# Optimization experiments

Hardware: AMD Instinct MI355X
Metric: run time of the kernel (lower is better)

## Reference

```python
import jax, jax.numpy as jnp
import numpy as np

B, N, F_IN = 512, 128, 133
NHID, NHEADS, HID = 64, 8, 512
FP_DIM, FP2, TASKS = 1489, 512, 12
ALPHA = 0.2
NEG_BIG = -9e15


def _lin_init(key, fan_in, fan_out):
    return jax.random.normal(key, (fan_in, fan_out), jnp.float32) / np.sqrt(fan_in)


def setup_inputs() -> dict:
    key = jax.random.key(0)
    ks = jax.random.split(key, 24)
    inp = {
        'h': jax.random.normal(ks[0], (B, N, F_IN), jnp.float32),
        'adj': jax.random.randint(ks[1], (B, N, N), 0, 2, jnp.int32),
        'edge_feat': jax.random.uniform(ks[2], (B, N, N), jnp.float32),
        'fp': jax.random.uniform(ks[3], (B, FP_DIM), jnp.float32),
        # multi-head GAT layer params (a split as [a1; a2; a_edge])
        'W_heads': jax.random.normal(ks[4], (NHEADS, F_IN, NHID), jnp.float32) / np.sqrt(F_IN),
        'a1_heads': jax.random.normal(ks[5], (NHEADS, NHID), jnp.float32) / np.sqrt(NHID),
        'a2_heads': jax.random.normal(ks[6], (NHEADS, NHID), jnp.float32) / np.sqrt(NHID),
        'ae_heads': jax.random.normal(ks[7], (NHEADS,), jnp.float32) * 0.1,
        # output GAT layer
        'W_out': jax.random.normal(ks[8], (NHID * NHEADS, HID), jnp.float32) / np.sqrt(NHID * NHEADS),
        'a1_out': jax.random.normal(ks[9], (HID,), jnp.float32) / np.sqrt(HID),
        'a2_out': jax.random.normal(ks[10], (HID,), jnp.float32) / np.sqrt(HID),
        'ae_out': jax.random.normal(ks[11], ()) * 0.1,
        # FPN
        'fc1_w': _lin_init(ks[12], FP_DIM, FP2), 'fc1_b': jnp.zeros((FP2,), jnp.float32),
        'fc2_w': _lin_init(ks[13], FP2, HID), 'fc2_b': jnp.zeros((HID,), jnp.float32),
        # cross-attention fusion
        'q_w': _lin_init(ks[14], HID, HID), 'q_b': jnp.zeros((HID,), jnp.float32),
        'k_w': _lin_init(ks[15], HID, HID), 'k_b': jnp.zeros((HID,), jnp.float32),
        'v_w': _lin_init(ks[16], HID, HID), 'v_b': jnp.zeros((HID,), jnp.float32),
        'o_w': _lin_init(ks[17], HID, HID), 'o_b': jnp.zeros((HID,), jnp.float32),
        # FFN head
        'ffn1_w': _lin_init(ks[18], HID, HID), 'ffn1_b': jnp.zeros((HID,), jnp.float32),
        'ffn2_w': _lin_init(ks[19], HID, TASKS), 'ffn2_b': jnp.zeros((TASKS,), jnp.float32),
    }
    return inp


def _leaky(x):
    return jnp.where(x >= 0, x, ALPHA * x)


def _fpgnn_forward(h, adj, edge_feat, fp,
                   W_heads, a1_heads, a2_heads, ae_heads,
                   W_out, a1_out, a2_out, ae_out,
                   fc1_w, fc1_b, fc2_w, fc2_b,
                   q_w, q_b, k_w, k_b, v_w, v_b, o_w, o_b,
                   ffn1_w, ffn1_b, ffn2_w, ffn2_b):
    mask = adj > 0  # [B,N,N]
    # --- multi-head GAT layers (concat=True) ---
    Wh = jnp.einsum('bnf,hfd->bhnd', h, W_heads)            # [B,H,N,D]
    s1 = jnp.einsum('bhnd,hd->bhn', Wh, a1_heads)
    s2 = jnp.einsum('bhnd,hd->bhn', Wh, a2_heads)
    # e[b,h,i,j] = leaky(Wh_i.a1 + Wh_j.a2 + edge_ij*ae)  (exact decomposition of
    # the original concat([Wh_i, Wh_j, edge_ij]) @ a)
    e = _leaky(s1[:, :, :, None] + s2[:, :, None, :]
               + edge_feat[:, None, :, :] * ae_heads[None, :, None, None])
    att = jnp.where(mask[:, None], e, NEG_BIG)
    att = jax.nn.softmax(att, axis=-1)                       # softmax over dim=1 of [N,N]
    hp = jnp.einsum('bhij,bhjd->bhid', att, Wh)
    x = jax.nn.elu(hp)                                       # concat=True -> ELU
    x = jnp.transpose(x, (0, 2, 1, 3)).reshape(B, N, NHEADS * NHID)
    # --- output GAT layer (concat=False) ---
    Wx = x @ W_out                                           # [B,N,HID]
    t1 = Wx @ a1_out                                         # [B,N]
    t2 = Wx @ a2_out
    e2 = _leaky(t1[:, :, None] + t2[:, None, :] + edge_feat * ae_out)
    att2 = jnp.where(mask, e2, NEG_BIG)
    att2 = jax.nn.softmax(att2, axis=-1)
    hp2 = jnp.einsum('bij,bjd->bid', att2, Wx)
    gat_nodes = jax.nn.elu(hp2)                              # F.elu in GATOne
    gat_out = gat_nodes.mean(axis=1)                         # molecule readout [B,HID]
    # --- FPN ---
    fpn_out = jax.nn.relu(fp @ fc1_w + fc1_b) @ fc2_w + fc2_b  # [B,HID]
    # --- cross-attention fusion ---
    q = gat_out @ q_w + q_b
    k = fpn_out @ k_w + k_b
    v = fpn_out @ v_w + v_b
    score = jnp.sum(q * k, axis=-1, keepdims=True) / np.sqrt(HID)  # [B,1]
    weight = jax.nn.softmax(score[:, :, None], axis=-1)[:, :, 0]    # softmax over size-1 dim -> ones
    fused = q + weight * v
    fused = jax.nn.relu(fused @ o_w + o_b)
    # --- FFN head (dropout p=0, eval) ---
    out = jax.nn.relu(fused @ ffn1_w + ffn1_b) @ ffn2_w + ffn2_b
    return out


def reference(h, adj, edge_feat, fp,
              W_heads, a1_heads, a2_heads, ae_heads,
              W_out, a1_out, a2_out, ae_out,
              fc1_w, fc1_b, fc2_w, fc2_b,
              q_w, q_b, k_w, k_b, v_w, v_b, o_w, o_b,
              ffn1_w, ffn1_b, ffn2_w, ffn2_b):
    return _fpgnn_forward(h, adj, edge_feat, fp,
                          W_heads, a1_heads, a2_heads, ae_heads,
                          W_out, a1_out, a2_out, ae_out,
                          fc1_w, fc1_b, fc2_w, fc2_b,
                          q_w, q_b, k_w, k_b, v_w, v_b, o_w, o_b,
                          ffn1_w, ffn1_b, ffn2_w, ffn2_b)
```

## Files before the change

kernel.cpp:

```cpp
#include <hip/hip_runtime.h>
#include <hip/hip_bf16.h>


#define ALPHA_LK 0.2f
#define LOG2E 1.44269504f
#define KP1 192
#define KPF 1536
#define MINF_BF16 0xFF80u

typedef unsigned short ushort_t;
typedef __attribute__((ext_vector_type(8))) short bfrag;
typedef __attribute__((ext_vector_type(4))) float ffrag;

__device__ __forceinline__ float b2f(ushort_t u) {
  return __uint_as_float(((unsigned)u) << 16);
}
__device__ __forceinline__ ushort_t f2b(float f) {
  unsigned u = __float_as_uint(f);
  unsigned r = (u + 0x7fffu + ((u >> 16) & 1u)) >> 16;
  return (ushort_t)r;
}
__device__ __forceinline__ unsigned cvt_pk(float lo, float hi) {
  unsigned r;
  asm("v_cvt_pk_bf16_f32 %0, %1, %2" : "=v"(r) : "v"(lo), "v"(hi));
  return r;
}
__device__ __forceinline__ float frcp(float x) {
  float r;
  asm("v_rcp_f32 %0, %1" : "=v"(r) : "v"(x));
  return r;
}
__device__ __forceinline__ float fexp2(float x) {
#if __has_builtin(__builtin_amdgcn_exp2f)
  return __builtin_amdgcn_exp2f(x);
#else
  return exp2f(x);
#endif
}
__device__ __forceinline__ float elu1(float v) {
  return v > 0.f ? v : __expf(v) - 1.f;
}

__device__ __forceinline__ void gll16(const void* g, void* l) {
  __builtin_amdgcn_global_load_lds(
      (const __attribute__((address_space(1))) unsigned int*)(unsigned long long)g,
      (__attribute__((address_space(3))) unsigned int*)(unsigned long long)l,
      16, 0, 0);
}

__global__ __launch_bounds__(256) void repack_h(const float* __restrict__ h,
                                                ushort_t* __restrict__ hb) {
  int o = blockIdx.x * 256 + threadIdx.x;
  int row = o / 48, c4 = (o - row * 48) * 4;
  const float* hr = h + (size_t)row * 133;
  ushort4 v;
  v.x = (c4 + 0 < 133) ? f2b(hr[c4 + 0]) : (ushort_t)0;
  v.y = (c4 + 1 < 133) ? f2b(hr[c4 + 1]) : (ushort_t)0;
  v.z = (c4 + 2 < 133) ? f2b(hr[c4 + 2]) : (ushort_t)0;
  v.w = (c4 + 3 < 133) ? f2b(hr[c4 + 3]) : (ushort_t)0;
  *(ushort4*)&hb[(size_t)row * KP1 + c4] = v;
}

__global__ __launch_bounds__(256) void repack_fp(const float* __restrict__ fp,
                                                 ushort_t* __restrict__ fpb) {
  int o = blockIdx.x * 256 + threadIdx.x;
  int row = o / 384, c4 = (o - row * 384) * 4;
  const float* fr = fp + (size_t)row * 1489;
  ushort4 v;
  v.x = (c4 + 0 < 1489) ? f2b(fr[c4 + 0]) : (ushort_t)0;
  v.y = (c4 + 1 < 1489) ? f2b(fr[c4 + 1]) : (ushort_t)0;
  v.z = (c4 + 2 < 1489) ? f2b(fr[c4 + 2]) : (ushort_t)0;
  v.w = (c4 + 3 < 1489) ? f2b(fr[c4 + 3]) : (ushort_t)0;
  *(ushort4*)&fpb[(size_t)row * KPF + c4] = v;
}

__global__ __launch_bounds__(256) void repack_w2t(const float* __restrict__ Whd,
                                                  ushort_t* __restrict__ W2t) {
  int o = blockIdx.x * 256 + threadIdx.x;
  if (o >= 512 * 48) return;
  int col = o / 48, c4 = (o - col * 48) * 4;
  int hh = col >> 6, d = col & 63;
  ushort4 v;
  v.x = (c4 + 0 < 133) ? f2b(Whd[(hh * 133 + c4 + 0) * 64 + d]) : (ushort_t)0;
  v.y = (c4 + 1 < 133) ? f2b(Whd[(hh * 133 + c4 + 1) * 64 + d]) : (ushort_t)0;
  v.z = (c4 + 2 < 133) ? f2b(Whd[(hh * 133 + c4 + 2) * 64 + d]) : (ushort_t)0;
  v.w = (c4 + 3 < 133) ? f2b(Whd[(hh * 133 + c4 + 3) * 64 + d]) : (ushort_t)0;
  *(ushort4*)&W2t[(size_t)col * KP1 + c4] = v;
}

__global__ __launch_bounds__(256) void repack_t(const float* __restrict__ W,
                                                ushort_t* __restrict__ Wt,
                                                int K, int N, int Kpad) {
  int kp4 = Kpad >> 2;
  int o = blockIdx.x * 256 + threadIdx.x;
  if (o >= N * kp4) return;
  int col = o / kp4, k4 = (o - col * kp4) * 4;
  ushort4 v;
  v.x = (k4 + 0 < K) ? f2b(W[(size_t)(k4 + 0) * N + col]) : (ushort_t)0;
  v.y = (k4 + 1 < K) ? f2b(W[(size_t)(k4 + 1) * N + col]) : (ushort_t)0;
  v.z = (k4 + 2 < K) ? f2b(W[(size_t)(k4 + 2) * N + col]) : (ushort_t)0;
  v.w = (k4 + 3 < K) ? f2b(W[(size_t)(k4 + 3) * N + col]) : (ushort_t)0;
  *(ushort4*)&Wt[(size_t)col * Kpad + k4] = v;
}

__global__ __launch_bounds__(256) void repack_t7(
    const float* __restrict__ w0, const float* __restrict__ w1,
    const float* __restrict__ w2, const float* __restrict__ w3,
    const float* __restrict__ w4, const float* __restrict__ w5,
    const float* __restrict__ qb, const float* __restrict__ vb,
    ushort_t* __restrict__ d0, ushort_t* __restrict__ d1,
    ushort_t* __restrict__ d2, ushort_t* __restrict__ d3,
    ushort_t* __restrict__ d4, ushort_t* __restrict__ d5,
    float* __restrict__ qvb) {
  int y = blockIdx.y;
  int o = blockIdx.x * 256 + threadIdx.x;
  if (y == 6) {
    if (o < 512) qvb[o] = qb[o] + vb[o];
    return;
  }
  const float* W = y == 0 ? w0 : y == 1 ? w1 : y == 2 ? w2
                 : y == 3 ? w3 : y == 4 ? w4 : w5;
  ushort_t* Wt = y == 0 ? d0 : y == 1 ? d1 : y == 2 ? d2
               : y == 3 ? d3 : y == 4 ? d4 : d5;
  int col = o >> 7, k4 = (o & 127) * 4;
  ushort4 v;
  v.x = f2b(W[(size_t)(k4 + 0) * 512 + col]);
  v.y = f2b(W[(size_t)(k4 + 1) * 512 + col]);
  v.z = f2b(W[(size_t)(k4 + 2) * 512 + col]);
  v.w = f2b(W[(size_t)(k4 + 3) * 512 + col]);
  *(ushort4*)&Wt[(size_t)col * 512 + k4] = v;
}

__global__ __launch_bounds__(256) void repack_em(const float* __restrict__ edge,
                                                 const int* __restrict__ adj,
                                                 ushort_t* __restrict__ em) {
  size_t o = ((size_t)blockIdx.x * 256 + threadIdx.x) * 4;
  float4 e = *(const float4*)&edge[o];
  int4 a = *(const int4*)&adj[o];
  ushort4 v;
  v.x = a.x > 0 ? f2b(e.x) : (ushort_t)MINF_BF16;
  v.y = a.y > 0 ? f2b(e.y) : (ushort_t)MINF_BF16;
  v.z = a.z > 0 ? f2b(e.z) : (ushort_t)MINF_BF16;
  v.w = a.w > 0 ? f2b(e.w) : (ushort_t)MINF_BF16;
  *(ushort4*)&em[o] = v;
}

__global__ __launch_bounds__(256) void wa12_kernel(
    const float* __restrict__ W, const float* __restrict__ a1,
    const float* __restrict__ a2, float* __restrict__ wa1,
    float* __restrict__ wa2) {
  int wv = threadIdx.x >> 6, lane = threadIdx.x & 63;
  int k = blockIdx.x * 4 + wv;
  const float* wr = W + (size_t)k * 512;
  float p1 = 0.f, p2 = 0.f;
#pragma unroll
  for (int i = 0; i < 8; ++i) {
    float v = wr[lane + i * 64];
    p1 += v * a1[lane + i * 64];
    p2 += v * a2[lane + i * 64];
  }
#pragma unroll
  for (int off = 32; off; off >>= 1) {
    p1 += __shfl_down(p1, off);
    p2 += __shfl_down(p2, off);
  }
  if (lane == 0) { wa1[k] = p1; wa2[k] = p2; }
}

__global__ __launch_bounds__(256) void t12x_kernel(
    const ushort_t* __restrict__ xb, const float* __restrict__ wa1,
    const float* __restrict__ wa2, float* __restrict__ t1o,
    float* __restrict__ t2o, int base) {
  int wv = threadIdx.x >> 6, lane = threadIdx.x & 63;
  int row = blockIdx.x * 4 + wv;
  const ushort_t* xr = xb + (size_t)row * 512;
  ushort4 u0 = *(const ushort4*)&xr[lane * 8];
  ushort4 u1 = *(const ushort4*)&xr[lane * 8 + 4];
  float xv[8] = {b2f(u0.x), b2f(u0.y), b2f(u0.z), b2f(u0.w),
                 b2f(u1.x), b2f(u1.y), b2f(u1.z), b2f(u1.w)};
  float p1 = 0.f, p2 = 0.f;
#pragma unroll
  for (int i = 0; i < 8; ++i) {
    p1 += xv[i] * wa1[lane * 8 + i];
    p2 += xv[i] * wa2[lane * 8 + i];
  }
#pragma unroll
  for (int off = 32; off; off >>= 1) {
    p1 += __shfl_down(p1, off);
    p2 += __shfl_down(p2, off);
  }
  if (lane == 0) {
    t1o[base * 128 + row] = p1;
    t2o[base * 128 + row] = p2;
  }
}

__global__ __launch_bounds__(256) void att2_kernel(
    const ushort_t* __restrict__ em, const float* __restrict__ t1,
    const float* __restrict__ t2, const float* __restrict__ aeo,
    ushort_t* __restrict__ awg, float* __restrict__ sinvg, int base) {
  __shared__ float t2s[128];
  const int bl = blockIdx.x >> 1, bg = base + bl;
  const int rb = (blockIdx.x & 1) * 64;
  const int t = threadIdx.x;
  if (t < 128) t2s[t] = t2[(size_t)bg * 128 + t] * LOG2E;
  __syncthreads();
  const int row = rb + (t >> 2), qtr = t & 3;
  const float ae2 = aeo[0] * LOG2E;
  const float rt1 = t1[(size_t)bg * 128 + row] * LOG2E;
  const ushort_t* emr = em + (size_t)bg * 16384 + row * 128 + qtr * 32;
  ushort_t* awr = awg + (size_t)bl * 16384 + row * 128 + qtr * 32;
  float s = 0.f;
#pragma unroll
  for (int v = 0; v < 4; ++v) {
    uint4 eu = *(const uint4*)&emr[v * 8];
    const unsigned uu[4] = {eu.x, eu.y, eu.z, eu.w};
    unsigned po[4];
#pragma unroll
    for (int pr = 0; pr < 4; ++pr) {
      float elo = __uint_as_float(uu[pr] << 16);
      float ehi = __uint_as_float(uu[pr] & 0xffff0000u);
      float e0 = fmaf(elo, ae2, rt1 + t2s[qtr * 32 + v * 8 + pr * 2]);
      float e1 = fmaf(ehi, ae2, rt1 + t2s[qtr * 32 + v * 8 + pr * 2 + 1]);
      e0 = fmaxf(e0, ALPHA_LK * e0);
      e1 = fmaxf(e1, ALPHA_LK * e1);
      float p0 = (elo != -INFINITY) ? fexp2(e0) : 0.f;
      float p1 = (ehi != -INFINITY) ? fexp2(e1) : 0.f;
      unsigned q = cvt_pk(p0, p1);
      po[pr] = q;
      s += __uint_as_float(q << 16) + __uint_as_float(q & 0xffff0000u);
    }
    *(uint4*)&awr[v * 8] = make_uint4(po[0], po[1], po[2], po[3]);
  }
  s += __shfl_xor(s, 1);
  s += __shfl_xor(s, 2);
  if (qtr == 0) sinvg[(size_t)bl * 128 + row] = 1.f / fmaxf(s, 1e-30f);
}

__global__ __launch_bounds__(256) void fused_gat1(
    const ushort_t* __restrict__ hb, const ushort_t* __restrict__ W2t,
    const ushort_t* __restrict__ edgeM, const float* __restrict__ a1h,
    const float* __restrict__ a2h, const float* __restrict__ ae,
    ushort_t* __restrict__ x, int base) {
  __shared__ union {
    struct { ushort_t As[128][64]; ushort_t Bs[64][64]; } g;
    ushort_t WS[64][136];
  } u;
  __shared__ float ss1[128], ss2[128];
  const int id = blockIdx.x;
  const int hh = (id >> 3) & 7;
  const int bl = ((id >> 6) << 3) | (id & 7);
  const int bg = base + bl;
  const int t = threadIdx.x;
  const int lane = t & 63, w = t >> 6;
  const int l16 = lane & 15, quad = lane >> 4;
  const int w8 = w * 8, sr8 = (t >> 3) & 7;
  const int csw = ((t & 7) ^ sr8) << 3;

  const ushort_t* gA = hb + (size_t)(bl * 128 + w8 + sr8) * KP1 + csw;
  const ushort_t* gB = W2t + (size_t)(hh * 64 + w8 + sr8) * KP1 + csw;
  ffrag acc[2][4];
#pragma unroll
  for (int mi = 0; mi < 2; ++mi)
#pragma unroll
    for (int ni = 0; ni < 4; ++ni) acc[mi][ni] = {0.f, 0.f, 0.f, 0.f};
  for (int k0 = 0; k0 < KP1; k0 += 64) {
    __syncthreads();
#pragma unroll
    for (int p = 0; p < 4; ++p)
      gll16(gA + (size_t)(p * 32) * KP1 + k0, &u.g.As[p * 32 + w8][0]);
#pragma unroll
    for (int p = 0; p < 2; ++p)
      gll16(gB + (size_t)(p * 32) * KP1 + k0, &u.g.Bs[p * 32 + w8][0]);
    __syncthreads();
#pragma unroll
    for (int ks = 0; ks < 2; ++ks) {
      const int cs = ((ks * 4 + quad) ^ (l16 & 7)) << 3;
      bfrag af[2], bf[4];
#pragma unroll
      for (int mi = 0; mi < 2; ++mi)
        af[mi] = *(const bfrag*)&u.g.As[w * 32 + mi * 16 + l16][cs];
#pragma unroll
      for (int ni = 0; ni < 4; ++ni)
        bf[ni] = *(const bfrag*)&u.g.Bs[ni * 16 + l16][cs];
#pragma unroll
      for (int mi = 0; mi < 2; ++mi)
#pragma unroll
        for (int ni = 0; ni < 4; ++ni)
          acc[mi][ni] = __builtin_amdgcn_mfma_f32_16x16x32_bf16(
              af[mi], bf[ni], acc[mi][ni], 0, 0, 0);
    }
  }
  __syncthreads();

#pragma unroll
  for (int mi = 0; mi < 2; ++mi)
#pragma unroll
    for (int ni = 0; ni < 4; ++ni) {
      int col = ni * 16 + l16;
      int rowb = w * 32 + mi * 16 + quad * 4;
      uint2 pv;
      pv.x = cvt_pk(acc[mi][ni][0], acc[mi][ni][1]);
      pv.y = cvt_pk(acc[mi][ni][2], acc[mi][ni][3]);
      *(uint2*)&u.WS[col][rowb] = pv;
    }
  __syncthreads();

  uint4 ereg[2][4];
  {
    const ushort_t* em = edgeM + (size_t)bg * 16384;
#pragma unroll
    for (int mi = 0; mi < 2; ++mi) {
      int row = w * 32 + mi * 16 + l16;
#pragma unroll
      for (int ks = 0; ks < 4; ++ks)
        ereg[mi][ks] = *(const uint4*)&em[row * 128 + ks * 32 + quad * 8];
    }
  }
  {
    int n = t & 127;
    const float* av = (t < 128) ? a1h : a2h;
    float p = 0.f;
#pragma unroll 8
    for (int d = 0; d < 64; ++d) p += b2f(u.WS[d][n]) * av[hh * 64 + d];
    p *= LOG2E;
    if (t < 128) ss1[n] = p; else ss2[n] = p;
  }
  __syncthreads();

  const float aeh2 = ae[hh] * LOG2E;
  float rs1[2];
  rs1[0] = ss1[w * 32 + l16];
  rs1[1] = ss1[w * 32 + 16 + l16];
  uint4 aw[2][4];
#pragma unroll
  for (int mi = 0; mi < 2; ++mi) {
#pragma unroll
    for (int ks = 0; ks < 4; ++ks) {
      float s2v[8];
      *(float4*)&s2v[0] = *(const float4*)&ss2[ks * 32 + quad * 8];
      *(float4*)&s2v[4] = *(const float4*)&ss2[ks * 32 + quad * 8 + 4];
      const unsigned uu[4] = {ereg[mi][ks].x, ereg[mi][ks].y,
                              ereg[mi][ks].z, ereg[mi][ks].w};
      unsigned po[4];
#pragma unroll
      for (int pr = 0; pr < 4; ++pr) {
        float elo = __uint_as_float(uu[pr] << 16);
        float ehi = __uint_as_float(uu[pr] & 0xffff0000u);
        float e0 = fmaf(elo, aeh2, rs1[mi] + s2v[pr * 2]);
        float e1 = fmaf(ehi, aeh2, rs1[mi] + s2v[pr * 2 + 1]);
        e0 = fmaxf(e0, ALPHA_LK * e0);
        e1 = fmaxf(e1, ALPHA_LK * e1);
        float p0 = (elo != -INFINITY) ? fexp2(e0) : 0.f;
        float p1 = (ehi != -INFINITY) ? fexp2(e1) : 0.f;
        po[pr] = cvt_pk(p0, p1);
      }
      aw[mi][ks] = make_uint4(po[0], po[1], po[2], po[3]);
    }
  }

  bfrag bones;
#pragma unroll
  for (int i = 0; i < 8; ++i) bones[i] = (short)0x3F80;

  ffrag acc2[2][4];
  ffrag accs[2];
#pragma unroll
  for (int mi = 0; mi < 2; ++mi) {
    accs[mi] = {0.f, 0.f, 0.f, 0.f};
#pragma unroll
    for (int ni = 0; ni < 4; ++ni) acc2[mi][ni] = {0.f, 0.f, 0.f, 0.f};
  }
#pragma unroll
  for (int ks = 0; ks < 4; ++ks) {
    bfrag bfr[4];
#pragma unroll
    for (int ni = 0; ni < 4; ++ni)
      bfr[ni] = *(const bfrag*)&u.WS[ni * 16 + l16][ks * 32 + quad * 8];
#pragma unroll
    for (int mi = 0; mi < 2; ++mi) {
      bfrag afr;
      __builtin_memcpy(&afr, &aw[mi][ks], 16);
#pragma unroll
      for (int ni = 0; ni < 4; ++ni)
        acc2[mi][ni] = __builtin_amdgcn_mfma_f32_16x16x32_bf16(
            afr, bfr[ni], acc2[mi][ni], 0, 0, 0);
      accs[mi] = __builtin_amdgcn_mfma_f32_16x16x32_bf16(
          afr, bones, accs[mi], 0, 0, 0);
    }
  }
  float sv[2][4];
#pragma unroll
  for (int mi = 0; mi < 2; ++mi)
#pragma unroll
    for (int r = 0; r < 4; ++r)
      sv[mi][r] = frcp(fmaxf(accs[mi][r], 1e-30f));

#pragma unroll
  for (int mi = 0; mi < 2; ++mi)
#pragma unroll
    for (int ni = 0; ni < 4; ++ni) {
      float e0 = elu1(acc2[mi][ni][0] * sv[mi][0]);
      float e1 = elu1(acc2[mi][ni][1] * sv[mi][1]);
      float e2 = elu1(acc2[mi][ni][2] * sv[mi][2]);
      float e3 = elu1(acc2[mi][ni][3] * sv[mi][3]);
      unsigned p01 = cvt_pk(e0, e1), p23 = cvt_pk(e2, e3);
      int rl = w * 32 + mi * 16 + quad * 4;
      size_t bo = (size_t)(bl * 128 + rl) * 512 + hh * 64 + ni * 16 + l16;
      x[bo] = (ushort_t)p01;
      x[bo + 512] = (ushort_t)(p01 >> 16);
      x[bo + 1024] = (ushort_t)p23;
      x[bo + 1536] = (ushort_t)(p23 >> 16);
    }
}

__global__ __launch_bounds__(256) void fused_gat2(
    const ushort_t* __restrict__ xb, const ushort_t* __restrict__ Wot,
    const ushort_t* __restrict__ awg, const float* __restrict__ sinvg,
    ushort_t* __restrict__ gatb, int base) {
  __shared__ union {
    struct { ushort_t As[128][64]; ushort_t Bs[128][64]; } g;
    ushort_t WS[128][136];
  } u;
  __shared__ float ps[4][64];
  const int id = blockIdx.x;
  const int sp2 = (id >> 3) & 3;
  const int bl = ((id >> 5) << 3) | (id & 7);
  const int bg = base + bl;
  const int t = threadIdx.x;
  const int lane = t & 63, w = t >> 6;
  const int wm = w >> 1, wn = w & 1;
  const int l16 = lane & 15, quad = lane >> 4;
  const int w8 = w * 8, sr8 = (t >> 3) & 7;
  const int csw = ((t & 7) ^ sr8) << 3;

  const ushort_t* gA = xb + (size_t)(bl * 128 + w8 + sr8) * 512 + csw;
  const ushort_t* gB = Wot + (size_t)(sp2 * 128 + w8 + sr8) * 512 + csw;
  ffrag acc[4][4];
#pragma unroll
  for (int mi = 0; mi < 4; ++mi)
#pragma unroll
    for (int ni = 0; ni < 4; ++ni) acc[mi][ni] = {0.f, 0.f, 0.f, 0.f};
  for (int k0 = 0; k0 < 512; k0 += 64) {
    __syncthreads();
#pragma unroll
    for (int p = 0; p < 4; ++p) {
      gll16(gA + (size_t)(p * 32) * 512 + k0, &u.g.As[p * 32 + w8][0]);
      gll16(gB + (size_t)(p * 32) * 512 + k0, &u.g.Bs[p * 32 + w8][0]);
    }
    __syncthreads();
#pragma unroll
    for (int ks = 0; ks < 2; ++ks) {
      const int cs = ((ks * 4 + quad) ^ (l16 & 7)) << 3;
      bfrag af[4], bf[4];
#pragma unroll
      for (int i = 0; i < 4; ++i) {
        af[i] = *(const bfrag*)&u.g.As[wm * 64 + i * 16 + l16][cs];
        bf[i] = *(const bfrag*)&u.g.Bs[wn * 64 + i * 16 + l16][cs];
      }
#pragma unroll
      for (int mi = 0; mi < 4; ++mi)
#pragma unroll
        for (int ni = 0; ni < 4; ++ni)
          acc[mi][ni] = __builtin_amdgcn_mfma_f32_16x16x32_bf16(
              af[mi], bf[ni], acc[mi][ni], 0, 0, 0);
    }
  }
  __syncthreads();

#pragma unroll
  for (int mi = 0; mi < 4; ++mi)
#pragma unroll
    for (int ni = 0; ni < 4; ++ni) {
      int col = wn * 64 + ni * 16 + l16;
      int rowb = wm * 64 + mi * 16 + quad * 4;
      uint2 pv;
      pv.x = cvt_pk(acc[mi][ni][0], acc[mi][ni][1]);
      pv.y = cvt_pk(acc[mi][ni][2], acc[mi][ni][3]);
      *(uint2*)&u.WS[col][rowb] = pv;
    }
  __syncthreads();

  uint4 awf[2][4];
  float sv[2][4];
  {
    const ushort_t* ap = awg + (size_t)bl * 16384;
#pragma unroll
    for (int mi = 0; mi < 2; ++mi) {
      int row = w * 32 + mi * 16 + l16;
#pragma unroll
      for (int ks = 0; ks < 4; ++ks)
        awf[mi][ks] = *(const uint4*)&ap[row * 128 + ks * 32 + quad * 8];
      float si = sinvg[(size_t)bl * 128 + row];
#pragma unroll
      for (int r = 0; r < 4; ++r) sv[mi][r] = __shfl(si, quad * 4 + r);
    }
  }

  for (int s0 = 0; s0 < 2; ++s0) {
    ffrag acc2[2][4];
#pragma unroll
    for (int mi = 0; mi < 2; ++mi)
#pragma unroll
      for (int ni = 0; ni < 4; ++ni) acc2[mi][ni] = {0.f, 0.f, 0.f, 0.f};
#pragma unroll
    for (int ks = 0; ks < 4; ++ks) {
      bfrag bfr[4];
#pragma unroll
      for (int ni = 0; ni < 4; ++ni)
        bfr[ni] = *(const bfrag*)&u.WS[s0 * 64 + ni * 16 + l16][ks * 32 + quad * 8];
#pragma unroll
      for (int mi = 0; mi < 2; ++mi) {
        bfrag afr;
        __builtin_memcpy(&afr, &awf[mi][ks], 16);
#pragma unroll
        for (int ni = 0; ni < 4; ++ni)
          acc2[mi][ni] = __builtin_amdgcn_mfma_f32_16x16x32_bf16(
              afr, bfr[ni], acc2[mi][ni], 0, 0, 0);
      }
    }
    __syncthreads();
#pragma unroll
    for (int ni = 0; ni < 4; ++ni) {
      float s = 0.f;
#pragma unroll
      for (int mi = 0; mi < 2; ++mi)
#pragma unroll
        for (int r = 0; r < 4; ++r) s += elu1(acc2[mi][ni][r] * sv[mi][r]);
      s += __shfl_xor(s, 16);
      s += __shfl_xor(s, 32);
      if (quad == 0) ps[w][ni * 16 + l16] = s;
    }
    __syncthreads();
    if (t < 64) {
      float s = ps[0][t] + ps[1][t] + ps[2][t] + ps[3][t];
      gatb[(size_t)bg * 512 + sp2 * 128 + s0 * 64 + t] = f2b(s * (1.f / 128.f));
    }
  }
}

__device__ __forceinline__ void tail_kloop(
    const ushort_t* __restrict__ A, const ushort_t* __restrict__ Bt,
    int K, int ld, ushort_t (*As)[64], ushort_t (*Bs)[64],
    ffrag (*acc)[4], int row0, int col0, int t) {
  const int lane = t & 63, w = t >> 6;
  const int wm = w >> 1, wn = w & 1;
  const int l16 = lane & 15, quad = lane >> 4;
  const int w8 = w * 8, sr8 = (t >> 3) & 7;
  const int csw = ((t & 7) ^ sr8) << 3;
  const ushort_t* gA = A + (size_t)(row0 + w8 + sr8) * ld + csw;
  const ushort_t* gB = Bt + (size_t)(col0 + w8 + sr8) * ld + csw;
  for (int k0 = 0; k0 < K; k0 += 64) {
    __syncthreads();
#pragma unroll
    for (int p = 0; p < 4; ++p) {
      gll16(gA + (size_t)(p * 32) * ld + k0, &As[p * 32 + w8][0]);
      gll16(gB + (size_t)(p * 32) * ld + k0, &Bs[p * 32 + w8][0]);
    }
    __syncthreads();
#pragma unroll
    for (int ks = 0; ks < 2; ++ks) {
      const int cs = ((ks * 4 + quad) ^ (l16 & 7)) << 3;
      bfrag af[4], bf[4];
#pragma unroll
      for (int i = 0; i < 4; ++i) {
        af[i] = *(const bfrag*)&As[wm * 64 + i * 16 + l16][cs];
        bf[i] = *(const bfrag*)&Bs[wn * 64 + i * 16 + l16][cs];
      }
#pragma unroll
      for (int mi = 0; mi < 4; ++mi)
#pragma unroll
        for (int ni = 0; ni < 4; ++ni)
          acc[mi][ni] = __builtin_amdgcn_mfma_f32_16x16x32_bf16(
              af[mi], bf[ni], acc[mi][ni], 0, 0, 0);
    }
  }
}

template <int DUAL, int RELU>
__global__ __launch_bounds__(256) void gemm_tail(
    const ushort_t* __restrict__ A1, const ushort_t* __restrict__ Bt1,
    int K1, int ld1,
    const ushort_t* __restrict__ A2, const ushort_t* __restrict__ Bt2,
    const float* __restrict__ bias, ushort_t* __restrict__ C) {
  __shared__ ushort_t As[128][64];
  __shared__ ushort_t Bs[128][64];
  const int t = threadIdx.x;
  const int lane = t & 63, w = t >> 6;
  const int wm = w >> 1, wn = w & 1;
  const int l16 = lane & 15, quad = lane >> 4;
  const int row0 = blockIdx.y * 128, col0 = blockIdx.x * 128;

  ffrag acc[4][4];
#pragma unroll
  for (int mi = 0; mi < 4; ++mi)
#pragma unroll
    for (int ni = 0; ni < 4; ++ni) acc[mi][ni] = {0.f, 0.f, 0.f, 0.f};

  tail_kloop(A1, Bt1, K1, ld1, As, Bs, acc, row0, col0, t);
  if (DUAL) tail_kloop(A2, Bt2, 512, 512, As, Bs, acc, row0, col0, t);

#pragma unroll
  for (int mi = 0; mi < 4; ++mi)
#pragma unroll
    for (int ni = 0; ni < 4; ++ni) {
      int col = col0 + wn * 64 + ni * 16 + l16;
      float bb = bias[col];
      float v0 = acc[mi][ni][0] + bb, v1 = acc[mi][ni][1] + bb;
      float v2 = acc[mi][ni][2] + bb, v3 = acc[mi][ni][3] + bb;
      if (RELU) {
        v0 = fmaxf(v0, 0.f); v1 = fmaxf(v1, 0.f);
        v2 = fmaxf(v2, 0.f); v3 = fmaxf(v3, 0.f);
      }
      unsigned p01 = cvt_pk(v0, v1), p23 = cvt_pk(v2, v3);
      int row = row0 + wm * 64 + mi * 16 + quad * 4;
      size_t o = (size_t)row * 512 + col;
      C[o] = (ushort_t)p01;
      C[o + 512] = (ushort_t)(p01 >> 16);
      C[o + 1024] = (ushort_t)p23;
      C[o + 1536] = (ushort_t)(p23 >> 16);
    }
}

__global__ __launch_bounds__(256) void ffn2_kernel(
    const ushort_t* __restrict__ f5, const float* __restrict__ W,
    const float* __restrict__ b, float* __restrict__ out) {
  int wv = threadIdx.x >> 6, lane = threadIdx.x & 63;
  int row = blockIdx.x * 4 + wv;
  const ushort_t* fr = f5 + (size_t)row * 512;
  float v[8];
  ushort4 u0 = *(const ushort4*)&fr[lane * 8];
  ushort4 u1 = *(const ushort4*)&fr[lane * 8 + 4];
  v[0] = b2f(u0.x); v[1] = b2f(u0.y); v[2] = b2f(u0.z); v[3] = b2f(u0.w);
  v[4] = b2f(u1.x); v[5] = b2f(u1.y); v[6] = b2f(u1.z); v[7] = b2f(u1.w);
#pragma unroll
  for (int j = 0; j < 12; ++j) {
    float s = 0.f;
#pragma unroll
    for (int i = 0; i < 8; ++i) s += v[i] * W[(size_t)(lane * 8 + i) * 12 + j];
#pragma unroll
    for (int off = 32; off; off >>= 1) s += __shfl_down(s, off);
    if (lane == 0) out[(size_t)row * 12 + j] = s + b[j];
  }
}

extern "C" void kernel_launch(void* const* d_in, const int* in_sizes, int n_in,
                              void* d_out, int out_size, void* d_ws, size_t ws_size,
                              hipStream_t stream) {
  const float* h        = (const float*)d_in[0];
  const int*   adj      = (const int*)d_in[1];
  const float* edge     = (const float*)d_in[2];
  const float* fp       = (const float*)d_in[3];
  const float* W_heads  = (const float*)d_in[4];
  const float* a1_heads = (const float*)d_in[5];
  const float* a2_heads = (const float*)d_in[6];
  const float* ae_heads = (const float*)d_in[7];
  const float* W_out  = (const float*)d_in[8];
  const float* a1_out = (const float*)d_in[9];
  const float* a2_out = (const float*)d_in[10];
  const float* ae_out = (const float*)d_in[11];
  const float* fc1_w = (const float*)d_in[12];
  const float* fc1_b = (const float*)d_in[13];
  const float* fc2_w = (const float*)d_in[14];
  const float* fc2_b = (const float*)d_in[15];
  const float* q_w = (const float*)d_in[16];
  const float* q_b = (const float*)d_in[17];
  const float* v_w = (const float*)d_in[20];
  const float* v_b = (const float*)d_in[21];
  const float* o_w = (const float*)d_in[22];
  const float* o_b = (const float*)d_in[23];
  const float* ffn1_w = (const float*)d_in[24];
  const float* ffn1_b = (const float*)d_in[25];
  const float* ffn2_w = (const float*)d_in[26];
  const float* ffn2_b = (const float*)d_in[27];
  float* out = (float*)d_out;

  const size_t hb_bytes = (size_t)65536 * KP1 * 2;
  const size_t em_bytes = (size_t)512 * 16384 * 2;
  const size_t tail_bytes =
      (size_t)512 * KPF * 2 * 2 + (size_t)512 * 512 * 2 * 12 + 2048;
  const size_t fixed_bytes = hb_bytes + em_bytes + (size_t)512 * KP1 * 2 +
                             (size_t)2 * 65536 * 4 + tail_bytes + 16384;
  int C = 32;
  for (int cand = 512; cand >= 32; cand >>= 1) {
    size_t need = (size_t)cand * (131072 + 32768 + 512) + fixed_bytes;
    if (need <= ws_size) { C = cand; break; }
  }
  const int M = C * 128;

  char* p = (char*)d_ws;
  ushort_t* xb  = (ushort_t*)p; p += (size_t)C * 65536 * 2;
  ushort_t* awg = (ushort_t*)p; p += (size_t)C * 16384 * 2;
  float* sinv   = (float*)p;    p += (size_t)C * 128 * 4;
  ushort_t* hb  = (ushort_t*)p; p += hb_bytes;
  ushort_t* em  = (ushort_t*)p; p += em_bytes;
  ushort_t* W2t = (ushort_t*)p; p += (size_t)512 * KP1 * 2;
  float* t1 = (float*)p; p += 65536 * 4;
  float* t2 = (float*)p; p += 65536 * 4;
  ushort_t* fpb  = (ushort_t*)p; p += (size_t)512 * KPF * 2;
  ushort_t* fc1t = (ushort_t*)p; p += (size_t)512 * KPF * 2;
  ushort_t* Wot  = (ushort_t*)p; p += (size_t)512 * 512 * 2;
  ushort_t* fc2t = (ushort_t*)p; p += (size_t)512 * 512 * 2;
  ushort_t* qwt  = (ushort_t*)p; p += (size_t)512 * 512 * 2;
  ushort_t* vwt  = (ushort_t*)p; p += (size_t)512 * 512 * 2;
  ushort_t* owt  = (ushort_t*)p; p += (size_t)512 * 512 * 2;
  ushort_t* f1t  = (ushort_t*)p; p += (size_t)512 * 512 * 2;
  ushort_t* gatb = (ushort_t*)p; p += (size_t)512 * 512 * 2;
  ushort_t* fb1  = (ushort_t*)p; p += (size_t)512 * 512 * 2;
  ushort_t* fb2  = (ushort_t*)p; p += (size_t)512 * 512 * 2;
  ushort_t* fb3  = (ushort_t*)p; p += (size_t)512 * 512 * 2;
  ushort_t* fb4  = (ushort_t*)p; p += (size_t)512 * 512 * 2;
  ushort_t* fb5  = (ushort_t*)p; p += (size_t)512 * 512 * 2;
  float* qvb = (float*)p; p += 2048;
  float* wa1 = (float*)p; p += 2048;
  float* wa2 = (float*)p; p += 2048;

  repack_h<<<12288, 256, 0, stream>>>(h, hb);
  repack_em<<<8192, 256, 0, stream>>>(edge, adj, em);
  repack_w2t<<<96, 256, 0, stream>>>(W_heads, W2t);
  repack_fp<<<768, 256, 0, stream>>>(fp, fpb);
  repack_t<<<768, 256, 0, stream>>>(fc1_w, fc1t, 1489, 512, KPF);
  repack_t7<<<dim3(256, 7), 256, 0, stream>>>(
      W_out, fc2_w, q_w, v_w, o_w, ffn1_w, q_b, v_b,
      Wot, fc2t, qwt, vwt, owt, f1t, qvb);
  wa12_kernel<<<128, 256, 0, stream>>>(W_out, a1_out, a2_out, wa1, wa2);

  for (int base = 0; base < 512; base += C) {
    fused_gat1<<<8 * C, 256, 0, stream>>>(
        hb + (size_t)base * 128 * KP1, W2t, em, a1_heads, a2_heads,
        ae_heads, xb, base);
    t12x_kernel<<<M / 4, 256, 0, stream>>>(xb, wa1, wa2, t1, t2, base);
    att2_kernel<<<2 * C, 256, 0, stream>>>(em, t1, t2, ae_out, awg, sinv, base);
    fused_gat2<<<4 * C, 256, 0, stream>>>(xb, Wot, awg, sinv, gatb, base);
  }

  gemm_tail<0, 1><<<dim3(4, 4), 256, 0, stream>>>(
      fpb, fc1t, KPF, KPF, nullptr, nullptr, fc1_b, fb1);
  gemm_tail<0, 0><<<dim3(4, 4), 256, 0, stream>>>(
      fb1, fc2t, 512, 512, nullptr, nullptr, fc2_b, fb2);
  gemm_tail<1, 0><<<dim3(4, 4), 256, 0, stream>>>(
      gatb, qwt, 512, 512, fb2, vwt, qvb, fb3);
  gemm_tail<0, 1><<<dim3(4, 4), 256, 0, stream>>>(
      fb3, owt, 512, 512, nullptr, nullptr, o_b, fb4);
  gemm_tail<0, 1><<<dim3(4, 4), 256, 0, stream>>>(
      fb4, f1t, 512, 512, nullptr, nullptr, ffn1_b, fb5);
  ffn2_kernel<<<128, 256, 0, stream>>>(fb5, ffn2_w, ffn2_b, out);
}
```

Baseline: 461.0 us.

## Merge prep kernels, fold attention projections into MFMA, fuse t12 into att2

All repack and weight-prep kernels become a single prep_all launch dispatched by block index. The layer-1 attention scores now come from an extra MFMA column built from W·a1 and W·a2, which are precomputed and stored as bf16. This replaces the per-thread post-GEMM dot products over the bf16 output tile. The t1/t2 projection kernel is fused into the layer-2 attention kernel, which removes launches and a global round trip. The costs are one block per graph in att2t, which gives less parallelism, and some precision loss because the folded attention vectors are rounded to bf16.

```diff
diff --git a/kernel.cpp b/kernel.cpp
--- a/kernel.cpp
+++ b/kernel.cpp
@@ -48,171 +48,199 @@
       16, 0, 0);
 }
 
-__global__ __launch_bounds__(256) void repack_h(const float* __restrict__ h,
-                                                ushort_t* __restrict__ hb) {
-  int o = blockIdx.x * 256 + threadIdx.x;
-  int row = o / 48, c4 = (o - row * 48) * 4;
-  const float* hr = h + (size_t)row * 133;
-  ushort4 v;
-  v.x = (c4 + 0 < 133) ? f2b(hr[c4 + 0]) : (ushort_t)0;
-  v.y = (c4 + 1 < 133) ? f2b(hr[c4 + 1]) : (ushort_t)0;
-  v.z = (c4 + 2 < 133) ? f2b(hr[c4 + 2]) : (ushort_t)0;
-  v.w = (c4 + 3 < 133) ? f2b(hr[c4 + 3]) : (ushort_t)0;
-  *(ushort4*)&hb[(size_t)row * KP1 + c4] = v;
-}
-
-__global__ __launch_bounds__(256) void repack_fp(const float* __restrict__ fp,
-                                                 ushort_t* __restrict__ fpb) {
-  int o = blockIdx.x * 256 + threadIdx.x;
-  int row = o / 384, c4 = (o - row * 384) * 4;
-  const float* fr = fp + (size_t)row * 1489;
-  ushort4 v;
-  v.x = (c4 + 0 < 1489) ? f2b(fr[c4 + 0]) : (ushort_t)0;
-  v.y = (c4 + 1 < 1489) ? f2b(fr[c4 + 1]) : (ushort_t)0;
-  v.z = (c4 + 2 < 1489) ? f2b(fr[c4 + 2]) : (ushort_t)0;
-  v.w = (c4 + 3 < 1489) ? f2b(fr[c4 + 3]) : (ushort_t)0;
-  *(ushort4*)&fpb[(size_t)row * KPF + c4] = v;
-}
-
-__global__ __launch_bounds__(256) void repack_w2t(const float* __restrict__ Whd,
-                                                  ushort_t* __restrict__ W2t) {
-  int o = blockIdx.x * 256 + threadIdx.x;
-  if (o >= 512 * 48) return;
-  int col = o / 48, c4 = (o - col * 48) * 4;
-  int hh = col >> 6, d = col & 63;
-  ushort4 v;
-  v.x = (c4 + 0 < 133) ? f2b(Whd[(hh * 133 + c4 + 0) * 64 + d]) : (ushort_t)0;
-  v.y = (c4 + 1 < 133) ? f2b(Whd[(hh * 133 + c4 + 1) * 64 + d]) : (ushort_t)0;
-  v.z = (c4 + 2 < 133) ? f2b(Whd[(hh * 133 + c4 + 2) * 64 + d]) : (ushort_t)0;
-  v.w = (c4 + 3 < 133) ? f2b(Whd[(hh * 133 + c4 + 3) * 64 + d]) : (ushort_t)0;
-  *(ushort4*)&W2t[(size_t)col * KP1 + c4] = v;
-}
-
-__global__ __launch_bounds__(256) void repack_t(const float* __restrict__ W,
-                                                ushort_t* __restrict__ Wt,
-                                                int K, int N, int Kpad) {
-  int kp4 = Kpad >> 2;
-  int o = blockIdx.x * 256 + threadIdx.x;
-  if (o >= N * kp4) return;
-  int col = o / kp4, k4 = (o - col * kp4) * 4;
-  ushort4 v;
-  v.x = (k4 + 0 < K) ? f2b(W[(size_t)(k4 + 0) * N + col]) : (ushort_t)0;
-  v.y = (k4 + 1 < K) ? f2b(W[(size_t)(k4 + 1) * N + col]) : (ushort_t)0;
-  v.z = (k4 + 2 < K) ? f2b(W[(size_t)(k4 + 2) * N + col]) : (ushort_t)0;
-  v.w = (k4 + 3 < K) ? f2b(W[(size_t)(k4 + 3) * N + col]) : (ushort_t)0;
-  *(ushort4*)&Wt[(size_t)col * Kpad + k4] = v;
-}
-
-__global__ __launch_bounds__(256) void repack_t7(
-    const float* __restrict__ w0, const float* __restrict__ w1,
-    const float* __restrict__ w2, const float* __restrict__ w3,
-    const float* __restrict__ w4, const float* __restrict__ w5,
+__global__ __launch_bounds__(256) void prep_all(
+    const float* __restrict__ h, const int* __restrict__ adj,
+    const float* __restrict__ edge, const float* __restrict__ fp,
+    const float* __restrict__ Whd, const float* __restrict__ a1h,
+    const float* __restrict__ a2h,
+    const float* __restrict__ W_out, const float* __restrict__ a1o,
+    const float* __restrict__ a2o,
+    const float* __restrict__ fc1_w, const float* __restrict__ fc2_w,
+    const float* __restrict__ q_w, const float* __restrict__ v_w,
+    const float* __restrict__ o_w, const float* __restrict__ ffn1_w,
     const float* __restrict__ qb, const float* __restrict__ vb,
-    ushort_t* __restrict__ d0, ushort_t* __restrict__ d1,
-    ushort_t* __restrict__ d2, ushort_t* __restrict__ d3,
-    ushort_t* __restrict__ d4, ushort_t* __restrict__ d5,
-    float* __restrict__ qvb) {
-  int y = blockIdx.y;
-  int o = blockIdx.x * 256 + threadIdx.x;
-  if (y == 6) {
-    if (o < 512) qvb[o] = qb[o] + vb[o];
+    ushort_t* __restrict__ hb, ushort_t* __restrict__ em,
+    ushort_t* __restrict__ W2t, ushort_t* __restrict__ fpb,
+    ushort_t* __restrict__ fc1t,
+    ushort_t* __restrict__ Wot, ushort_t* __restrict__ fc2t,
+    ushort_t* __restrict__ qwt, ushort_t* __restrict__ vwt,
+    ushort_t* __restrict__ owt, ushort_t* __restrict__ f1t,
+    float* __restrict__ wa1, float* __restrict__ wa2,
+    ushort_t* __restrict__ wh12, float* __restrict__ qvb) {
+  int bid = blockIdx.x;
+  const int t = threadIdx.x;
+
+  if (bid < 8) {
+    int hh = bid;
+    if (t < 192) {
+      float s1 = 0.f, s2 = 0.f;
+      if (t < 133) {
+        const float* wr = Whd + (size_t)(hh * 133 + t) * 64;
+        const float* a1r = a1h + hh * 64;
+        const float* a2r = a2h + hh * 64;
+#pragma unroll 8
+        for (int d = 0; d < 64; ++d) {
+          float wv = wr[d];
+          s1 += wv * a1r[d];
+          s2 += wv * a2r[d];
+        }
+      }
+      wh12[hh * 384 + t] = f2b(s1);
+      wh12[hh * 384 + 192 + t] = f2b(s2);
+    }
     return;
   }
-  const float* W = y == 0 ? w0 : y == 1 ? w1 : y == 2 ? w2
-                 : y == 3 ? w3 : y == 4 ? w4 : w5;
-  ushort_t* Wt = y == 0 ? d0 : y == 1 ? d1 : y == 2 ? d2
-               : y == 3 ? d3 : y == 4 ? d4 : d5;
-  int col = o >> 7, k4 = (o & 127) * 4;
-  ushort4 v;
-  v.x = f2b(W[(size_t)(k4 + 0) * 512 + col]);
-  v.y = f2b(W[(size_t)(k4 + 1) * 512 + col]);
-  v.z = f2b(W[(size_t)(k4 + 2) * 512 + col]);
-  v.w = f2b(W[(size_t)(k4 + 3) * 512 + col]);
-  *(ushort4*)&Wt[(size_t)col * 512 + k4] = v;
-}
-
-__global__ __launch_bounds__(256) void repack_em(const float* __restrict__ edge,
-                                                 const int* __restrict__ adj,
-                                                 ushort_t* __restrict__ em) {
-  size_t o = ((size_t)blockIdx.x * 256 + threadIdx.x) * 4;
-  float4 e = *(const float4*)&edge[o];
-  int4 a = *(const int4*)&adj[o];
-  ushort4 v;
-  v.x = a.x > 0 ? f2b(e.x) : (ushort_t)MINF_BF16;
-  v.y = a.y > 0 ? f2b(e.y) : (ushort_t)MINF_BF16;
-  v.z = a.z > 0 ? f2b(e.z) : (ushort_t)MINF_BF16;
-  v.w = a.w > 0 ? f2b(e.w) : (ushort_t)MINF_BF16;
-  *(ushort4*)&em[o] = v;
-}
-
-__global__ __launch_bounds__(256) void wa12_kernel(
-    const float* __restrict__ W, const float* __restrict__ a1,
-    const float* __restrict__ a2, float* __restrict__ wa1,
-    float* __restrict__ wa2) {
-  int wv = threadIdx.x >> 6, lane = threadIdx.x & 63;
-  int k = blockIdx.x * 4 + wv;
-  const float* wr = W + (size_t)k * 512;
-  float p1 = 0.f, p2 = 0.f;
-#pragma unroll
-  for (int i = 0; i < 8; ++i) {
-    float v = wr[lane + i * 64];
-    p1 += v * a1[lane + i * 64];
-    p2 += v * a2[lane + i * 64];
-  }
-#pragma unroll
-  for (int off = 32; off; off >>= 1) {
-    p1 += __shfl_down(p1, off);
-    p2 += __shfl_down(p2, off);
-  }
-  if (lane == 0) { wa1[k] = p1; wa2[k] = p2; }
-}
-
-__global__ __launch_bounds__(256) void t12x_kernel(
-    const ushort_t* __restrict__ xb, const float* __restrict__ wa1,
-    const float* __restrict__ wa2, float* __restrict__ t1o,
-    float* __restrict__ t2o, int base) {
-  int wv = threadIdx.x >> 6, lane = threadIdx.x & 63;
-  int row = blockIdx.x * 4 + wv;
-  const ushort_t* xr = xb + (size_t)row * 512;
-  ushort4 u0 = *(const ushort4*)&xr[lane * 8];
-  ushort4 u1 = *(const ushort4*)&xr[lane * 8 + 4];
-  float xv[8] = {b2f(u0.x), b2f(u0.y), b2f(u0.z), b2f(u0.w),
-                 b2f(u1.x), b2f(u1.y), b2f(u1.z), b2f(u1.w)};
-  float p1 = 0.f, p2 = 0.f;
-#pragma unroll
-  for (int i = 0; i < 8; ++i) {
-    p1 += xv[i] * wa1[lane * 8 + i];
-    p2 += xv[i] * wa2[lane * 8 + i];
-  }
-#pragma unroll
-  for (int off = 32; off; off >>= 1) {
-    p1 += __shfl_down(p1, off);
-    p2 += __shfl_down(p2, off);
-  }
-  if (lane == 0) {
-    t1o[base * 128 + row] = p1;
-    t2o[base * 128 + row] = p2;
-  }
-}
-
-__global__ __launch_bounds__(256) void att2_kernel(
-    const ushort_t* __restrict__ em, const float* __restrict__ t1,
-    const float* __restrict__ t2, const float* __restrict__ aeo,
+  bid -= 8;
+  if (bid < 128) {
+    int wv = t >> 6, lane = t & 63;
+    int k = bid * 4 + wv;
+    const float* wr = W_out + (size_t)k * 512;
+    float p1 = 0.f, p2 = 0.f;
+#pragma unroll
+    for (int i = 0; i < 8; ++i) {
+      float v = wr[lane + i * 64];
+      p1 += v * a1o[lane + i * 64];
+      p2 += v * a2o[lane + i * 64];
+    }
+#pragma unroll
+    for (int off = 32; off; off >>= 1) {
+      p1 += __shfl_down(p1, off);
+      p2 += __shfl_down(p2, off);
+    }
+    if (lane == 0) { wa1[k] = p1; wa2[k] = p2; }
+    return;
+  }
+  bid -= 128;
+  if (bid < 2) {
+    int o = bid * 256 + t;
+    qvb[o] = qb[o] + vb[o];
+    return;
+  }
+  bid -= 2;
+  if (bid < 96) {
+    int o = bid * 256 + t;
+    if (o < 512 * 48) {
+      int col = o / 48, c4 = (o - col * 48) * 4;
+      int hh = col >> 6, d = col & 63;
+      ushort4 v;
+      v.x = (c4 + 0 < 133) ? f2b(Whd[(hh * 133 + c4 + 0) * 64 + d]) : (ushort_t)0;
+      v.y = (c4 + 1 < 133) ? f2b(Whd[(hh * 133 + c4 + 1) * 64 + d]) : (ushort_t)0;
+      v.z = (c4 + 2 < 133) ? f2b(Whd[(hh * 133 + c4 + 2) * 64 + d]) : (ushort_t)0;
+      v.w = (c4 + 3 < 133) ? f2b(Whd[(hh * 133 + c4 + 3) * 64 + d]) : (ushort_t)0;
+      *(ushort4*)&W2t[(size_t)col * KP1 + c4] = v;
+    }
+    return;
+  }
+  bid -= 96;
+  if (bid < 768) {
+    int o = bid * 256 + t;
+    int row = o / 384, c4 = (o - row * 384) * 4;
+    const float* fr = fp + (size_t)row * 1489;
+    ushort4 v;
+    v.x = (c4 + 0 < 1489) ? f2b(fr[c4 + 0]) : (ushort_t)0;
+    v.y = (c4 + 1 < 1489) ? f2b(fr[c4 + 1]) : (ushort_t)0;
+    v.z = (c4 + 2 < 1489) ? f2b(fr[c4 + 2]) : (ushort_t)0;
+    v.w = (c4 + 3 < 1489) ? f2b(fr[c4 + 3]) : (ushort_t)0;
+    *(ushort4*)&fpb[(size_t)row * KPF + c4] = v;
+    return;
+  }
+  bid -= 768;
+  if (bid < 768) {
+    int o = bid * 256 + t;
+    int col = o / 384, k4 = (o - col * 384) * 4;
+    ushort4 v;
+    v.x = (k4 + 0 < 1489) ? f2b(fc1_w[(size_t)(k4 + 0) * 512 + col]) : (ushort_t)0;
+    v.y = (k4 + 1 < 1489) ? f2b(fc1_w[(size_t)(k4 + 1) * 512 + col]) : (ushort_t)0;
+    v.z = (k4 + 2 < 1489) ? f2b(fc1_w[(size_t)(k4 + 2) * 512 + col]) : (ushort_t)0;
+    v.w = (k4 + 3 < 1489) ? f2b(fc1_w[(size_t)(k4 + 3) * 512 + col]) : (ushort_t)0;
+    *(ushort4*)&fc1t[(size_t)col * KPF + k4] = v;
+    return;
+  }
+  bid -= 768;
+  if (bid < 1536) {
+    int y = bid >> 8;
+    int o = (bid & 255) * 256 + t;
+    const float* W = y == 0 ? W_out : y == 1 ? fc2_w : y == 2 ? q_w
+                   : y == 3 ? v_w : y == 4 ? o_w : ffn1_w;
+    ushort_t* Wt = y == 0 ? Wot : y == 1 ? fc2t : y == 2 ? qwt
+                 : y == 3 ? vwt : y == 4 ? owt : f1t;
+    int col = o >> 7, k4 = (o & 127) * 4;
+    ushort4 v;
+    v.x = f2b(W[(size_t)(k4 + 0) * 512 + col]);
+    v.y = f2b(W[(size_t)(k4 + 1) * 512 + col]);
+    v.z = f2b(W[(size_t)(k4 + 2) * 512 + col]);
+    v.w = f2b(W[(size_t)(k4 + 3) * 512 + col]);
+    *(ushort4*)&Wt[(size_t)col * 512 + k4] = v;
+    return;
+  }
+  bid -= 1536;
+  if (bid < 12288) {
+    int o = bid * 256 + t;
+    int row = o / 48, c4 = (o - row * 48) * 4;
+    const float* hr = h + (size_t)row * 133;
+    ushort4 v;
+    v.x = (c4 + 0 < 133) ? f2b(hr[c4 + 0]) : (ushort_t)0;
+    v.y = (c4 + 1 < 133) ? f2b(hr[c4 + 1]) : (ushort_t)0;
+    v.z = (c4 + 2 < 133) ? f2b(hr[c4 + 2]) : (ushort_t)0;
+    v.w = (c4 + 3 < 133) ? f2b(hr[c4 + 3]) : (ushort_t)0;
+    *(ushort4*)&hb[(size_t)row * KP1 + c4] = v;
+    return;
+  }
+  bid -= 12288;
+  {
+    size_t o = ((size_t)bid * 256 + t) * 4;
+    float4 e = *(const float4*)&edge[o];
+    int4 a = *(const int4*)&adj[o];
+    ushort4 v;
+    v.x = a.x > 0 ? f2b(e.x) : (ushort_t)MINF_BF16;
+    v.y = a.y > 0 ? f2b(e.y) : (ushort_t)MINF_BF16;
+    v.z = a.z > 0 ? f2b(e.z) : (ushort_t)MINF_BF16;
+    v.w = a.w > 0 ? f2b(e.w) : (ushort_t)MINF_BF16;
+    *(ushort4*)&em[o] = v;
+  }
+}
+
+__global__ __launch_bounds__(256) void att2t(
+    const ushort_t* __restrict__ xb, const ushort_t* __restrict__ em,
+    const float* __restrict__ wa1, const float* __restrict__ wa2,
+    const float* __restrict__ aeo,
     ushort_t* __restrict__ awg, float* __restrict__ sinvg, int base) {
-  __shared__ float t2s[128];
-  const int bl = blockIdx.x >> 1, bg = base + bl;
-  const int rb = (blockIdx.x & 1) * 64;
+  __shared__ float t1s[128], t2s[128];
+  __shared__ float was1[512], was2[512];
+  const int bl = blockIdx.x, bg = base + bl;
   const int t = threadIdx.x;
-  if (t < 128) t2s[t] = t2[(size_t)bg * 128 + t] * LOG2E;
+  was1[t] = wa1[t]; was1[t + 256] = wa1[t + 256];
+  was2[t] = wa2[t]; was2[t + 256] = wa2[t + 256];
   __syncthreads();
-  const int row = rb + (t >> 2), qtr = t & 3;
+  const int row = t >> 1, half = t & 1;
+  {
+    const ushort_t* xr = xb + (size_t)(bl * 128 + row) * 512 + half * 256;
+    float p1 = 0.f, p2 = 0.f;
+#pragma unroll 4
+    for (int i = 0; i < 32; ++i) {
+      uint4 u = *(const uint4*)&xr[i * 8];
+      const unsigned uu[4] = {u.x, u.y, u.z, u.w};
+#pragma unroll
+      for (int pr = 0; pr < 4; ++pr) {
+        float lo = __uint_as_float(uu[pr] << 16);
+        float hi = __uint_as_float(uu[pr] & 0xffff0000u);
+        int c = half * 256 + i * 8 + pr * 2;
+        p1 = fmaf(lo, was1[c], p1); p1 = fmaf(hi, was1[c + 1], p1);
+        p2 = fmaf(lo, was2[c], p2); p2 = fmaf(hi, was2[c + 1], p2);
+      }
+    }
+    p1 += __shfl_xor(p1, 1);
+    p2 += __shfl_xor(p2, 1);
+    if (!half) { t1s[row] = p1 * LOG2E; t2s[row] = p2 * LOG2E; }
+  }
+  __syncthreads();
   const float ae2 = aeo[0] * LOG2E;
-  const float rt1 = t1[(size_t)bg * 128 + row] * LOG2E;
-  const ushort_t* emr = em + (size_t)bg * 16384 + row * 128 + qtr * 32;
-  ushort_t* awr = awg + (size_t)bl * 16384 + row * 128 + qtr * 32;
+  const float rt1 = t1s[row];
+  const ushort_t* emr = em + (size_t)bg * 16384 + row * 128 + half * 64;
+  ushort_t* awr = awg + (size_t)bl * 16384 + row * 128 + half * 64;
   float s = 0.f;
 #pragma unroll
-  for (int v = 0; v < 4; ++v) {
+  for (int v = 0; v < 8; ++v) {
     uint4 eu = *(const uint4*)&emr[v * 8];
     const unsigned uu[4] = {eu.x, eu.y, eu.z, eu.w};
     unsigned po[4];
@@ -220,8 +248,8 @@
     for (int pr = 0; pr < 4; ++pr) {
       float elo = __uint_as_float(uu[pr] << 16);
       float ehi = __uint_as_float(uu[pr] & 0xffff0000u);
-      float e0 = fmaf(elo, ae2, rt1 + t2s[qtr * 32 + v * 8 + pr * 2]);
-      float e1 = fmaf(ehi, ae2, rt1 + t2s[qtr * 32 + v * 8 + pr * 2 + 1]);
+      float e0 = fmaf(elo, ae2, rt1 + t2s[half * 64 + v * 8 + pr * 2]);
+      float e1 = fmaf(ehi, ae2, rt1 + t2s[half * 64 + v * 8 + pr * 2 + 1]);
       e0 = fmaxf(e0, ALPHA_LK * e0);
       e1 = fmaxf(e1, ALPHA_LK * e1);
       float p0 = (elo != -INFINITY) ? fexp2(e0) : 0.f;
@@ -233,20 +261,20 @@
     *(uint4*)&awr[v * 8] = make_uint4(po[0], po[1], po[2], po[3]);
   }
   s += __shfl_xor(s, 1);
-  s += __shfl_xor(s, 2);
-  if (qtr == 0) sinvg[(size_t)bl * 128 + row] = 1.f / fmaxf(s, 1e-30f);
+  if (!half) sinvg[(size_t)bl * 128 + row] = 1.f / fmaxf(s, 1e-30f);
 }
 
 __global__ __launch_bounds__(256) void fused_gat1(
     const ushort_t* __restrict__ hb, const ushort_t* __restrict__ W2t,
-    const ushort_t* __restrict__ edgeM, const float* __restrict__ a1h,
-    const float* __restrict__ a2h, const float* __restrict__ ae,
+    const ushort_t* __restrict__ edgeM, const ushort_t* __restrict__ wh12g,
+    const float* __restrict__ ae,
     ushort_t* __restrict__ x, int base) {
   __shared__ union {
     struct { ushort_t As[128][64]; ushort_t Bs[64][64]; } g;
     ushort_t WS[64][136];
   } u;
   __shared__ float ss1[128], ss2[128];
+  __shared__ ushort_t wh12s[2][192];
   const int id = blockIdx.x;
   const int hh = (id >> 3) & 7;
   const int bl = ((id >> 6) << 3) | (id & 7);
@@ -257,13 +285,20 @@
   const int w8 = w * 8, sr8 = (t >> 3) & 7;
   const int csw = ((t & 7) ^ sr8) << 3;
 
+  if (t < 96)
+    *(ushort4*)&(&wh12s[0][0])[t * 4] =
+        *(const ushort4*)&wh12g[hh * 384 + t * 4];
+
   const ushort_t* gA = hb + (size_t)(bl * 128 + w8 + sr8) * KP1 + csw;
   const ushort_t* gB = W2t + (size_t)(hh * 64 + w8 + sr8) * KP1 + csw;
   ffrag acc[2][4];
-#pragma unroll
-  for (int mi = 0; mi < 2; ++mi)
+  ffrag acc_s[2];
+#pragma unroll
+  for (int mi = 0; mi < 2; ++mi) {
+    acc_s[mi] = {0.f, 0.f, 0.f, 0.f};
 #pragma unroll
     for (int ni = 0; ni < 4; ++ni) acc[mi][ni] = {0.f, 0.f, 0.f, 0.f};
+  }
   for (int k0 = 0; k0 < KP1; k0 += 64) {
     __syncthreads();
 #pragma unroll
@@ -277,6 +312,9 @@
     for (int ks = 0; ks < 2; ++ks) {
       const int cs = ((ks * 4 + quad) ^ (l16 & 7)) << 3;
       bfrag af[2], bf[4];
+      bfrag bs = {0, 0, 0, 0, 0, 0, 0, 0};
+      if (l16 < 2)
+        bs = *(const bfrag*)&wh12s[l16][k0 + ks * 32 + quad * 8];
 #pragma unroll
       for (int mi = 0; mi < 2; ++mi)
         af[mi] = *(const bfrag*)&u.g.As[w * 32 + mi * 16 + l16][cs];
@@ -284,11 +322,14 @@
       for (int ni = 0; ni < 4; ++ni)
         bf[ni] = *(const bfrag*)&u.g.Bs[ni * 16 + l16][cs];
 #pragma unroll
-      for (int mi = 0; mi < 2; ++mi)
+      for (int mi = 0; mi < 2; ++mi) {
 #pragma unroll
         for (int ni = 0; ni < 4; ++ni)
           acc[mi][ni] = __builtin_amdgcn_mfma_f32_16x16x32_bf16(
               af[mi], bf[ni], acc[mi][ni], 0, 0, 0);
+        acc_s[mi] = __builtin_amdgcn_mfma_f32_16x16x32_bf16(
+            af[mi], bs, acc_s[mi], 0, 0, 0);
+      }
     }
   }
   __syncthreads();
@@ -304,8 +345,14 @@
       pv.y = cvt_pk(acc[mi][ni][2], acc[mi][ni][3]);
       *(uint2*)&u.WS[col][rowb] = pv;
     }
-  __syncthreads();
-
+  if (l16 < 2) {
+    float* sp = (l16 == 0) ? ss1 : ss2;
+#pragma unroll
+    for (int mi = 0; mi < 2; ++mi)
+#pragma unroll
+      for (int r = 0; r < 4; ++r)
+        sp[w * 32 + mi * 16 + quad * 4 + r] = acc_s[mi][r] * LOG2E;
+  }
   uint4 ereg[2][4];
   {
     const ushort_t* em = edgeM + (size_t)bg * 16384;
@@ -316,15 +363,6 @@
       for (int ks = 0; ks < 4; ++ks)
         ereg[mi][ks] = *(const uint4*)&em[row * 128 + ks * 32 + quad * 8];
     }
-  }
-  {
-    int n = t & 127;
-    const float* av = (t < 128) ? a1h : a2h;
-    float p = 0.f;
-#pragma unroll 8
-    for (int d = 0; d < 64; ++d) p += b2f(u.WS[d][n]) * av[hh * 64 + d];
-    p *= LOG2E;
-    if (t < 128) ss1[n] = p; else ss2[n] = p;
   }
   __syncthreads();
 
@@ -687,6 +725,7 @@
     if (need <= ws_size) { C = cand; break; }
   }
   const int M = C * 128;
+  (void)M;
 
   char* p = (char*)d_ws;
   ushort_t* xb  = (ushort_t*)p; p += (size_t)C * 65536 * 2;
@@ -695,8 +734,9 @@
   ushort_t* hb  = (ushort_t*)p; p += hb_bytes;
   ushort_t* em  = (ushort_t*)p; p += em_bytes;
   ushort_t* W2t = (ushort_t*)p; p += (size_t)512 * KP1 * 2;
-  float* t1 = (float*)p; p += 65536 * 4;
-  float* t2 = (float*)p; p += 65536 * 4;
+  ushort_t* wh12 = (ushort_t*)p; p += 8 * 384 * 2;
+  float* t_unused = (float*)p; p += 2 * 65536 * 4 - 8 * 384 * 2;
+  (void)t_unused;
   ushort_t* fpb  = (ushort_t*)p; p += (size_t)512 * KPF * 2;
   ushort_t* fc1t = (ushort_t*)p; p += (size_t)512 * KPF * 2;
   ushort_t* Wot  = (ushort_t*)p; p += (size_t)512 * 512 * 2;
@@ -715,22 +755,17 @@
   float* wa1 = (float*)p; p += 2048;
   float* wa2 = (float*)p; p += 2048;
 
-  repack_h<<<12288, 256, 0, stream>>>(h, hb);
-  repack_em<<<8192, 256, 0, stream>>>(edge, adj, em);
-  repack_w2t<<<96, 256, 0, stream>>>(W_heads, W2t);
-  repack_fp<<<768, 256, 0, stream>>>(fp, fpb);
-  repack_t<<<768, 256, 0, stream>>>(fc1_w, fc1t, 1489, 512, KPF);
-  repack_t7<<<dim3(256, 7), 256, 0, stream>>>(
-      W_out, fc2_w, q_w, v_w, o_w, ffn1_w, q_b, v_b,
-      Wot, fc2t, qwt, vwt, owt, f1t, qvb);
-  wa12_kernel<<<128, 256, 0, stream>>>(W_out, a1_out, a2_out, wa1, wa2);
+  prep_all<<<23786, 256, 0, stream>>>(
+      h, adj, edge, fp, W_heads, a1_heads, a2_heads,
+      W_out, a1_out, a2_out,
+      fc1_w, fc2_w, q_w, v_w, o_w, ffn1_w, q_b, v_b,
+      hb, em, W2t, fpb, fc1t, Wot, fc2t, qwt, vwt, owt, f1t,
+      wa1, wa2, wh12, qvb);
 
   for (int base = 0; base < 512; base += C) {
     fused_gat1<<<8 * C, 256, 0, stream>>>(
-        hb + (size_t)base * 128 * KP1, W2t, em, a1_heads, a2_heads,
-        ae_heads, xb, base);
-    t12x_kernel<<<M / 4, 256, 0, stream>>>(xb, wa1, wa2, t1, t2, base);
-    att2_kernel<<<2 * C, 256, 0, stream>>>(em, t1, t2, ae_out, awg, sinv, base);
+        hb + (size_t)base * 128 * KP1, W2t, em, wh12, ae_heads, xb, base);
+    att2t<<<C, 256, 0, stream>>>(xb, em, wa1, wa2, ae_out, awg, sinv, base);
     fused_gat2<<<4 * C, 256, 0, stream>>>(xb, Wot, awg, sinv, gatb, base);
   }
 
```

Measured after the change: 425.6 us (median of 3 runs). -7.7%, faster.
